# Optimization experiments

Measured on AMD Instinct MI355X. Metric: run time of the kernel, lower is better.

## Reference

```python
import jax, jax.numpy as jnp
import numpy as np

B, C, H, W = 32, 3, 64, 64
KH, KW = 3, 3


def setup_inputs() -> dict:
    key = jax.random.key(0)
    x = jax.random.normal(key, (B, C, H, W), dtype=jnp.float32)
    return {"x": x}


def reference(x):
    b, c, h, w = x.shape
    hout, wout = h - KH + 1, w - KW + 1
    # im2col / nn.Unfold: torch orders the D=C*KH*KW axis channel-major:
    # index = c*KH*KW + i*KW + j
    patches = jnp.stack(
        [x[:, :, i:i + hout, j:j + wout] for i in range(KH) for j in range(KW)],
        axis=2,
    )  # [B, C, KH*KW, Hout, Wout]
    D = c * KH * KW
    p = patches.reshape(b, D, hout * wout).transpose(0, 2, 1)  # [B, L, D]
    # torch.combinations(row, 2, with_replacement=True) enumerates pairs
    # (i, j) with i <= j in lexicographic order == upper triangle row-major.
    ti, tj = jnp.triu_indices(D)
    feats = p[:, :, ti] * p[:, :, tj]  # [B, L, D*(D+1)//2]
    return feats.reshape(b, -1)
```

## Files before the change

### kernel.cpp

```cpp
#include <hip/hip_runtime.h>


#define B_    32
#define C_    3
#define H_    64
#define W_    64
#define HOUT  62
#define WOUT  62
#define L_    (HOUT * WOUT)
#define D_    27
#define NPAIR 378
#define NPOS  (B_ * L_)

__global__ __launch_bounds__(256) void localde_kernel(
    const float* __restrict__ x, float* __restrict__ out) {
  const int tid  = threadIdx.x;
  const int lane = tid & 63;
  const int wv   = tid >> 6;
  const int half = lane >> 5;
  const int j    = lane & 31;
  const int jj   = (j < D_) ? j : (D_ - 1);

  const int pos = (blockIdx.x * 4 + wv) * 2 + half;
  int b  = pos / L_;
  int l  = pos - b * L_;
  int oh = l / WOUT;
  int ow = l - oh * WOUT;

  int c  = jj / 9;
  int r  = jj - c * 9;
  int ki = r / 3;
  int kj = r - ki * 3;

  const float pj  = x[((b * C_ + c) * H_ + oh + ki) * W_ + ow + kj];
  const int   pjb = __float_as_int(pj);

  float* const base = out + (size_t)pos * NPAIR + j;

#pragma unroll
  for (int i = 0; i < D_; ++i) {
    const int s = i * D_ - (i * (i - 1)) / 2;
    int lo = __builtin_amdgcn_readlane(pjb, i);
    int hi = __builtin_amdgcn_readlane(pjb, 32 + i);
    float pi = __int_as_float(half ? hi : lo);
    if (j >= i && j < D_) base[s - i] = pi * pj;
  }
}

extern "C" void kernel_launch(void* const* d_in, const int* in_sizes, int n_in,
                              void* d_out, int out_size, void* d_ws, size_t ws_size,
                              hipStream_t stream) {
  const float* x = (const float*)d_in[0];
  float* out = (float*)d_out;
  const int grid = NPOS / 8;
  localde_kernel<<<grid, 256, 0, stream>>>(x, out);
}
```

Before: 37.43 us.

## Stage input rows in LDS and emit vectorized float4 output per row

Each 64-thread block now handles one output row: it loads the 9 needed input rows into shared memory, then writes pairs of positions as contiguous float4 stores using precomputed pair-index offsets. The aim is to replace masked scalar stores and cross-lane readlane broadcasts with full-width vector stores. The trade-off is fewer waves per block and lower occupancy, which may limit how well memory latency is hidden.

```diff
diff --git a/kernel.cpp b/kernel.cpp
--- a/kernel.cpp
+++ b/kernel.cpp
@@ -10,40 +10,69 @@
 #define L_    (HOUT * WOUT)
 #define D_    27
 #define NPAIR 378
-#define NPOS  (B_ * L_)
+#define XSS   67
 
-__global__ __launch_bounds__(256) void localde_kernel(
+typedef float f32x4 __attribute__((ext_vector_type(4)));
+
+__global__ __launch_bounds__(64) void localde_kernel(
     const float* __restrict__ x, float* __restrict__ out) {
-  const int tid  = threadIdx.x;
-  const int lane = tid & 63;
-  const int wv   = tid >> 6;
-  const int half = lane >> 5;
-  const int j    = lane & 31;
-  const int jj   = (j < D_) ? j : (D_ - 1);
+  __shared__ float xs[9 * XSS];
 
-  const int pos = (blockIdx.x * 4 + wv) * 2 + half;
-  int b  = pos / L_;
-  int l  = pos - b * L_;
-  int oh = l / WOUT;
-  int ow = l - oh * WOUT;
-
-  int c  = jj / 9;
-  int r  = jj - c * 9;
-  int ki = r / 3;
-  int kj = r - ki * 3;
-
-  const float pj  = x[((b * C_ + c) * H_ + oh + ki) * W_ + ow + kj];
-  const int   pjb = __float_as_int(pj);
-
-  float* const base = out + (size_t)pos * NPAIR + j;
+  const int lane = threadIdx.x;
+  const int bo = blockIdx.x;
+  const int b  = bo / HOUT;
+  const int oh = bo - b * HOUT;
 
 #pragma unroll
-  for (int i = 0; i < D_; ++i) {
-    const int s = i * D_ - (i * (i - 1)) / 2;
-    int lo = __builtin_amdgcn_readlane(pjb, i);
-    int hi = __builtin_amdgcn_readlane(pjb, 32 + i);
-    float pi = __int_as_float(half ? hi : lo);
-    if (j >= i && j < D_) base[s - i] = pi * pj;
+  for (int t0 = 0; t0 < 3; ++t0) {
+    int t = lane + (t0 << 6);
+    if (t < 144) {
+      int row = t >> 4;
+      int c4  = (t & 15) << 2;
+      const float* src =
+          x + (((size_t)(b * C_ + row / 3) * H_) + oh + row % 3) * W_ + c4;
+      f32x4 v = *(const f32x4*)src;
+      float* dst = &xs[row * XSS + c4];
+      dst[0] = v[0]; dst[1] = v[1]; dst[2] = v[2]; dst[3] = v[3];
+    }
+  }
+  __syncthreads();
+
+  int offA[3][4], offB[3][4];
+#pragma unroll
+  for (int t = 0; t < 3; ++t) {
+#pragma unroll
+    for (int k = 0; k < 4; ++k) {
+      int e = 4 * (lane + (t << 6)) + k;
+      if (e > 755) e = 755;
+      int pos = (e >= NPAIR) ? 1 : 0;
+      int ee = e - pos * NPAIR;
+      int i = (int)((55.0f - sqrtf((float)(3025 - 8 * ee))) * 0.5f);
+      int j = ee - (27 * i - ((i * (i - 1)) >> 1)) + i;
+      offA[t][k] = ((i / 3) * XSS + (i % 3) + pos) * 4;
+      offB[t][k] = ((j / 3) * XSS + (j % 3) + pos) * 4;
+    }
+  }
+
+  float* orow = out + (size_t)(b * L_ + oh * WOUT) * NPAIR;
+  const char* xsb = (const char*)xs;
+
+  for (int s = 0; s < WOUT / 2; ++s) {
+    f32x4* op = (f32x4*)(orow + s * (2 * NPAIR));
+    const int so = s * 8;
+#pragma unroll
+    for (int t = 0; t < 3; ++t) {
+      if (t < 2 || lane < 61) {
+        f32x4 v;
+#pragma unroll
+        for (int k = 0; k < 4; ++k) {
+          float a = *(const float*)(xsb + offA[t][k] + so);
+          float c = *(const float*)(xsb + offB[t][k] + so);
+          v[k] = a * c;
+        }
+        op[lane + (t << 6)] = v;
+      }
+    }
   }
 }
 
@@ -52,6 +81,5 @@
                               hipStream_t stream) {
   const float* x = (const float*)d_in[0];
   float* out = (float*)d_out;
-  const int grid = NPOS / 8;
-  localde_kernel<<<grid, 256, 0, stream>>>(x, out);
+  localde_kernel<<<B_ * HOUT, 64, 0, stream>>>(x, out);
 }
```

Result: faster. 34.69 us (-7.3%).
